# Performance work log

Hardware: AMD Instinct MI355X
Metric: run time of the kernel (lower is better)

## Reference

```python
import jax, jax.numpy as jnp
import numpy as np

NEG_SLOPE = 0.2  # PyG GATConv default negative_slope


def gat_conv(x, W, a_src, a_dst, bias, src, dst, heads, out_c, concat):
    """PyG-style GATConv with self-loops. x:[N,F_in], W:[F_in,heads*out_c]."""
    N = x.shape[0]
    # add self loops
    loop = jnp.arange(N, dtype=src.dtype)
    src = jnp.concatenate([src, loop])
    dst = jnp.concatenate([dst, loop])
    h = (x @ W).reshape(N, heads, out_c)            # [N,H,C]
    alpha_src = jnp.sum(h * a_src, axis=-1)          # [N,H]
    alpha_dst = jnp.sum(h * a_dst, axis=-1)          # [N,H]
    e = jax.nn.leaky_relu(alpha_src[src] + alpha_dst[dst], NEG_SLOPE)  # [E,H]
    # segment softmax over incoming edges of each destination node
    m = jax.ops.segment_max(e, dst, num_segments=N)  # [N,H]
    ex = jnp.exp(e - m[dst])
    s = jax.ops.segment_sum(ex, dst, num_segments=N)
    alpha = ex / (s[dst] + 1e-16)                    # [E,H]
    msg = h[src] * alpha[:, :, None]                 # [E,H,C]
    out = jax.ops.segment_sum(msg, dst, num_segments=N)  # [N,H,C]
    out = out.reshape(N, heads * out_c) if concat else out.mean(axis=1)
    return out + bias


def setup_inputs() -> dict:
    key = jax.random.key(0)
    ks = jax.random.split(key, 16)
    N, E = 25000, 400000
    node_dim, hidden, out_dim, heads = 64, 128, 256, 4

    def glorot(k, shape):
        fan = shape[0] + shape[-1]
        return jax.random.normal(k, shape, jnp.float32) * np.sqrt(2.0 / fan)

    return {
        "x": jax.random.normal(ks[0], (N, node_dim), jnp.float32),
        "edge_index": jax.random.randint(ks[1], (2, E), 0, N, jnp.int32),
        "W_emb": glorot(ks[2], (node_dim, hidden)),
        "b_emb": jnp.zeros((hidden,), jnp.float32),
        "W1": glorot(ks[3], (hidden, heads * hidden)),
        "a1_src": glorot(ks[4], (heads, hidden)),
        "a1_dst": glorot(ks[5], (heads, hidden)),
        "b1": jnp.zeros((heads * hidden,), jnp.float32),
        "W2": glorot(ks[6], (heads * hidden, hidden)),
        "a2_src": glorot(ks[7], (1, hidden)),
        "a2_dst": glorot(ks[8], (1, hidden)),
        "b2": jnp.zeros((hidden,), jnp.float32),
        "W_out": glorot(ks[9], (hidden, out_dim)),
        "b_out": jnp.zeros((out_dim,), jnp.float32),
    }


def reference(x, edge_index, W_emb, b_emb, W1, a1_src, a1_dst, b1, W2, a2_src, a2_dst, b2, W_out, b_out):
    src, dst = edge_index[0], edge_index[1]
    heads, hidden = a1_src.shape[0], a1_src.shape[1]
    h = jax.nn.relu(x @ W_emb + b_emb)                 # dropout is identity in eval
    h = gat_conv(h, W1, a1_src, a1_dst, b1, src, dst, heads, hidden, True)
    h = jax.nn.elu(h)
    h = gat_conv(h, W2, a2_src, a2_dst, b2, src, dst, 1, hidden, False)
    h = jax.nn.elu(h)
    g = jnp.mean(h, axis=0, keepdims=True)             # global mean pool, batch=None -> [1, hidden]
    return g @ W_out + b_out                           # [1, out_dim]
```

## Files before the change

kernel.cpp:

```cpp
#include <hip/hip_runtime.h>
#include <hip/hip_bf16.h>


#define LRELU(x) ((x) > 0.f ? (x) : 0.2f * (x))

typedef short bf16x8 __attribute__((ext_vector_type(8)));
typedef float f32x4 __attribute__((ext_vector_type(4)));
typedef float f32x2 __attribute__((ext_vector_type(2)));

static __device__ __forceinline__ unsigned short f2b(float f) {
    union { float f; unsigned u; } x; x.f = f;
    unsigned r = x.u + 0x7fff + ((x.u >> 16) & 1);
    return (unsigned short)(r >> 16);
}
static __device__ __forceinline__ float rl_f(float v, int c) {
    return __int_as_float(__builtin_amdgcn_readlane(__float_as_int(v), c));
}
static __device__ __forceinline__ unsigned char f2fp8(float v) {
    int p = __builtin_amdgcn_cvt_pk_fp8_f32(v, v, 0, false);
    return (unsigned char)(p & 0xff);
}

__global__ void zero_kernel(int* __restrict__ deg, float* __restrict__ pool,
                            int* __restrict__ done, int* __restrict__ flg,
                            int* __restrict__ agg, int N, int nb) {
    int i = blockIdx.x * blockDim.x + threadIdx.x;
    if (i < N) { deg[i] = 0; return; }
    i -= N;
    if (i < 128) { pool[i] = 0.f; return; }
    i -= 128;
    if (i == 0) { *done = 0; return; }
    i -= 1;
    if (i < nb) { flg[i] = 0; return; }
    i -= nb;
    if (i < nb) agg[i] = 0;
}

__global__ void degcount_prep(const int* __restrict__ ei, int E, int N,
                              int* __restrict__ deg, int blocksE,
                              const float* __restrict__ x, const float* __restrict__ We,
                              const float* __restrict__ W1, const float* __restrict__ W2,
                              unsigned short* __restrict__ xbS, unsigned short* __restrict__ WeS,
                              unsigned short* __restrict__ W1S, unsigned short* __restrict__ W2T,
                              int Nx) {
    if ((int)blockIdx.x < blocksE) {
        int i = blockIdx.x * blockDim.x + threadIdx.x;
        if (i < E) atomicAdd(&deg[ei[E + i]], 1);
        else if (i < E + N) atomicAdd(&deg[i - E], 1);
        return;
    }
    int i = (blockIdx.x - blocksE) * blockDim.x + threadIdx.x;
    if (i < Nx) {
        int r = i >> 6, k = i & 63;
        xbS[(r >> 4) * 1024 + (k >> 3) * 128 + (r & 15) * 8 + (k & 7)] = f2b(x[i]);
        return;
    }
    i -= Nx;
    if (i < 64 * 128) {
        int k = i >> 7, n = i & 127;
        WeS[(n >> 4) * 1024 + (k >> 5) * 512 + ((k >> 3) & 3) * 128 + (n & 15) * 8 + (k & 7)] = f2b(We[i]);
        return;
    }
    i -= 64 * 128;
    if (i < 128 * 512) {
        int k = i >> 9, n = i & 511;
        W1S[(n >> 4) * 2048 + (k >> 5) * 512 + ((k >> 3) & 3) * 128 + (n & 15) * 8 + (k & 7)] = f2b(W1[i]);
        return;
    }
    i -= 128 * 512;
    if (i < 512 * 128) { int k = i >> 7, n = i & 127; W2T[n * 512 + k] = f2b(W2[i]); return; }
}

__global__ __launch_bounds__(256) void scan_lookback(const int* __restrict__ deg,
                                                     int* __restrict__ rowptr,
                                                     int* __restrict__ cursor,
                                                     int* __restrict__ agg,
                                                     int* __restrict__ flg,
                                                     int N, int nb) {
    __shared__ int sd[256];
    __shared__ int soff;
    int t = threadIdx.x, b = blockIdx.x;
    int i = b * 256 + t;
    int d = (i < N) ? deg[i] : 0;
    sd[t] = d;
    __syncthreads();
    for (int off = 1; off < 256; off <<= 1) {
        int v = (t >= off) ? sd[t - off] : 0;
        __syncthreads();
        sd[t] += v;
        __syncthreads();
    }
    int incl = sd[t];
    int btot = sd[255];
    if (t == 0) {
        soff = 0;
        __hip_atomic_store(&agg[b], btot, __ATOMIC_RELAXED, __HIP_MEMORY_SCOPE_AGENT);
        __hip_atomic_store(&flg[b], 1, __ATOMIC_RELEASE, __HIP_MEMORY_SCOPE_AGENT);
    }
    if (b > 0 && t < 64) {
        int acc = 0;
        for (int p = t; p < b; p += 64) {
            while (__hip_atomic_load(&flg[p], __ATOMIC_ACQUIRE, __HIP_MEMORY_SCOPE_AGENT) == 0)
                __builtin_amdgcn_s_sleep(1);
            acc += __hip_atomic_load(&agg[p], __ATOMIC_RELAXED, __HIP_MEMORY_SCOPE_AGENT);
        }
#pragma unroll
        for (int o = 32; o >= 1; o >>= 1) acc += __shfl_xor(acc, o);
        if (t == 0) soff = acc;
    }
    __syncthreads();
    int off = soff;
    int excl = off + incl - d;
    if (i < N) { rowptr[i] = excl; cursor[i] = excl; }
    if (b == nb - 1 && t == 255) rowptr[N] = off + btot;
}

__global__ void scatter_kernel(const int* __restrict__ ei, int E, int N,
                               int* __restrict__ cursor, int* __restrict__ esrc) {
    int i = blockIdx.x * blockDim.x + threadIdx.x;
    int s, d;
    if (i < E) { s = ei[i]; d = ei[E + i]; }
    else if (i < E + N) { s = i - E; d = s; }
    else return;
    int pos = atomicAdd(&cursor[d], 1);
    esrc[pos] = s;
}

__global__ __launch_bounds__(256, 3) void gemm12_fused(const unsigned short* __restrict__ xbS,
                                                       const unsigned short* __restrict__ WeS,
                                                       const float* __restrict__ b_emb,
                                                       const unsigned short* __restrict__ W1S,
                                                       unsigned char* __restrict__ C8,
                                                       const float* __restrict__ a_src,
                                                       const float* __restrict__ a_dst,
                                                       float* __restrict__ as_out,
                                                       float* __restrict__ ad_out, int M) {
    __shared__ __align__(16) unsigned short h0s[128 * 132];
    __shared__ float sAl[128][2];

    int tid = threadIdx.x;
    int bx = blockIdx.x, by = blockIdx.y;
    int gm0 = by * 128, gn0 = bx * 128;
    int w = tid >> 6, lane = tid & 63;
    int wrow = (w >> 1) * 64, wc = w & 1, wcol = wc * 64;
    int l15 = lane & 15, quad = lane >> 4;

    f32x4 acc[4][4];
#pragma unroll
    for (int i = 0; i < 4; i++)
#pragma unroll
        for (int j = 0; j < 4; j++) acc[i][j] = {0.f, 0.f, 0.f, 0.f};

    const unsigned short* xA = xbS + (size_t)((gm0 + wrow) >> 4) * 1024 + quad * 128 + l15 * 8;
    const unsigned short* wB = WeS + (size_t)(wc * 4) * 1024 + quad * 128 + l15 * 8;
    const unsigned short* w1B = W1S + (size_t)(bx * 8 + wc * 4) * 2048 + quad * 128 + l15 * 8;
#pragma unroll
    for (int ks = 0; ks < 2; ks++) {
        bf16x8 af[4], bfr[4];
#pragma unroll
        for (int i = 0; i < 4; i++) af[i] = *(const bf16x8*)(xA + i * 1024 + ks * 512);
#pragma unroll
        for (int j = 0; j < 4; j++) bfr[j] = *(const bf16x8*)(wB + j * 1024 + ks * 512);
#pragma unroll
        for (int i = 0; i < 4; i++)
#pragma unroll
            for (int j = 0; j < 4; j++)
                acc[i][j] = __builtin_amdgcn_mfma_f32_16x16x32_bf16(af[i], bfr[j], acc[i][j], 0, 0, 0);
    }

    bf16x8 wp[4][4];
#pragma unroll
    for (int ks = 0; ks < 4; ks++)
#pragma unroll
        for (int j = 0; j < 4; j++)
            wp[ks][j] = *(const bf16x8*)(w1B + j * 2048 + ks * 512);

#pragma unroll
    for (int j = 0; j < 4; j++) {
        int col = wcol + j * 16 + l15;
        float bv = b_emb[col];
#pragma unroll
        for (int i = 0; i < 4; i++) {
            int row = wrow + i * 16 + quad * 4;
#pragma unroll
            for (int r = 0; r < 4; r++) {
                float v = fmaxf(acc[i][j][r] + bv, 0.f);
                h0s[(row + r) * 132 + col] = f2b(v);
            }
        }
    }
#pragma unroll
    for (int i = 0; i < 4; i++)
#pragma unroll
        for (int j = 0; j < 4; j++) acc[i][j] = {0.f, 0.f, 0.f, 0.f};
    __syncthreads();

#pragma unroll
    for (int ks = 0; ks < 4; ks++) {
        bf16x8 af[4];
#pragma unroll
        for (int i = 0; i < 4; i++)
            af[i] = *(const bf16x8*)&h0s[(wrow + i * 16 + l15) * 132 + ks * 32 + quad * 8];
#pragma unroll
        for (int i = 0; i < 4; i++)
#pragma unroll
            for (int j = 0; j < 4; j++)
                acc[i][j] = __builtin_amdgcn_mfma_f32_16x16x32_bf16(af[i], wp[ks][j], acc[i][j], 0, 0, 0);
    }

#pragma unroll
    for (int i = 0; i < 4; i++) {
        int row = gm0 + wrow + i * 16 + quad * 4;
#pragma unroll
        for (int j = 0; j < 4; j++) {
            int col = gn0 + wcol + j * 16 + l15;
#pragma unroll
            for (int r = 0; r < 4; r++) {
                int gr = row + r;
                if (gr < M) C8[(size_t)gr * 512 + col] = f2fp8(acc[i][j][r]);
            }
        }
    }

    {
        int hh = bx;
        float as_c[4], ad_c[4];
#pragma unroll
        for (int j = 0; j < 4; j++) {
            int c = gn0 + wcol + j * 16 + l15;
            as_c[j] = a_src[c];
            ad_c[j] = a_dst[c];
        }
#pragma unroll
        for (int i = 0; i < 4; i++) {
#pragma unroll
            for (int r = 0; r < 4; r++) {
                float ps = 0.f, pd = 0.f;
#pragma unroll
                for (int j = 0; j < 4; j++) {
                    ps += acc[i][j][r] * as_c[j];
                    pd += acc[i][j][r] * ad_c[j];
                }
#pragma unroll
                for (int o = 1; o < 16; o <<= 1) {
                    ps += __shfl_xor(ps, o);
                    pd += __shfl_xor(pd, o);
                }
                if (wcol == 64 && l15 == 0) {
                    int lr = wrow + i * 16 + quad * 4 + r;
                    sAl[lr][0] = ps;
                    sAl[lr][1] = pd;
                }
            }
        }
        __syncthreads();
        if (wcol == 0) {
#pragma unroll
            for (int i = 0; i < 4; i++) {
#pragma unroll
                for (int r = 0; r < 4; r++) {
                    float ps = 0.f, pd = 0.f;
#pragma unroll
                    for (int j = 0; j < 4; j++) {
                        ps += acc[i][j][r] * as_c[j];
                        pd += acc[i][j][r] * ad_c[j];
                    }
#pragma unroll
                    for (int o = 1; o < 16; o <<= 1) {
                        ps += __shfl_xor(ps, o);
                        pd += __shfl_xor(pd, o);
                    }
                    if (l15 == 0) {
                        int lr = wrow + i * 16 + quad * 4 + r;
                        int gr = gm0 + lr;
                        if (gr < M) {
                            as_out[(size_t)gr * 4 + hh] = ps + sAl[lr][0];
                            ad_out[(size_t)gr * 4 + hh] = pd + sAl[lr][1];
                        }
                    }
                }
            }
        }
    }
}

template <int ACT, int OFMT, int ALPHA, int H>
__global__ __launch_bounds__(256) void gemm_mfma_nt(const unsigned short* __restrict__ A,
                                                    const unsigned short* __restrict__ Bt,
                                                    const float* __restrict__ bias,
                                                    void* __restrict__ Cout,
                                                    const float* __restrict__ a_src,
                                                    const float* __restrict__ a_dst,
                                                    float* __restrict__ as_out,
                                                    float* __restrict__ ad_out,
                                                    int M, int N, int K) {
    __shared__ __align__(16) unsigned short As[128 * 40];
    __shared__ __align__(16) unsigned short Bs[128 * 40];
    __shared__ float sAl[128][2];
    int tid = threadIdx.x;
    int gm0 = blockIdx.y * 128, gn0 = blockIdx.x * 128;
    int w = tid >> 6, lane = tid & 63;
    int wrow = (w >> 1) * 64, wcol = (w & 1) * 64;
    int l15 = lane & 15, quad = lane >> 4;

    f32x4 acc[4][4];
#pragma unroll
    for (int i = 0; i < 4; i++)
#pragma unroll
        for (int j = 0; j < 4; j++) acc[i][j] = {0.f, 0.f, 0.f, 0.f};

    for (int k0 = 0; k0 < K; k0 += 32) {
#pragma unroll
        for (int rr = 0; rr < 2; rr++) {
            int lin = tid + rr * 256;
            int row = lin >> 2;
            int cg = (lin & 3) * 8;
            int grow = gm0 + row; if (grow >= M) grow = M - 1;
            uint4 va = *(const uint4*)&A[(size_t)grow * K + k0 + cg];
            *(uint4*)&As[row * 40 + cg] = va;
            uint4 vb = *(const uint4*)&Bt[(size_t)(gn0 + row) * K + k0 + cg];
            *(uint4*)&Bs[row * 40 + cg] = vb;
        }
        __syncthreads();
        bf16x8 af[4], bfr[4];
#pragma unroll
        for (int i = 0; i < 4; i++) {
            af[i]  = *(const bf16x8*)&As[(wrow + i * 16 + l15) * 40 + quad * 8];
            bfr[i] = *(const bf16x8*)&Bs[(wcol + i * 16 + l15) * 40 + quad * 8];
        }
#pragma unroll
        for (int i = 0; i < 4; i++)
#pragma unroll
            for (int j = 0; j < 4; j++)
                acc[i][j] = __builtin_amdgcn_mfma_f32_16x16x32_bf16(af[i], bfr[j], acc[i][j], 0, 0, 0);
        __syncthreads();
    }

    if (OFMT == 0) {
        unsigned short* C = (unsigned short*)Cout;
#pragma unroll
        for (int i = 0; i < 4; i++) {
            int row = gm0 + wrow + i * 16 + quad * 4;
#pragma unroll
            for (int j = 0; j < 4; j++) {
                int col = gn0 + wcol + j * 16 + l15;
                float bv = bias ? bias[col] : 0.f;
#pragma unroll
                for (int r = 0; r < 4; r++) {
                    int gr = row + r;
                    if (gr < M) {
                        float v = acc[i][j][r] + bv;
                        if (ACT == 1) v = fmaxf(v, 0.f);
                        C[(size_t)gr * N + col] = f2b(v);
                    }
                }
            }
        }
    } else {
        unsigned char* C8 = (unsigned char*)Cout;
#pragma unroll
        for (int i = 0; i < 4; i++) {
            int row = gm0 + wrow + i * 16 + quad * 4;
#pragma unroll
            for (int j = 0; j < 4; j++) {
                int col = gn0 + wcol + j * 16 + l15;
#pragma unroll
                for (int r = 0; r < 4; r++) {
                    int gr = row + r;
                    if (gr < M) C8[(size_t)gr * N + col] = f2fp8(acc[i][j][r]);
                }
            }
        }
    }

    if (ALPHA) {
        int hh = blockIdx.x;
        float as_c[4], ad_c[4];
#pragma unroll
        for (int j = 0; j < 4; j++) {
            int c = gn0 + wcol + j * 16 + l15;
            as_c[j] = a_src[c];
            ad_c[j] = a_dst[c];
        }
#pragma unroll
        for (int i = 0; i < 4; i++) {
#pragma unroll
            for (int r = 0; r < 4; r++) {
                float ps = 0.f, pd = 0.f;
#pragma unroll
                for (int j = 0; j < 4; j++) {
                    ps += acc[i][j][r] * as_c[j];
                    pd += acc[i][j][r] * ad_c[j];
                }
#pragma unroll
                for (int o = 1; o < 16; o <<= 1) {
                    ps += __shfl_xor(ps, o);
                    pd += __shfl_xor(pd, o);
                }
                if (wcol == 64 && l15 == 0) {
                    int lr = wrow + i * 16 + quad * 4 + r;
                    sAl[lr][0] = ps;
                    sAl[lr][1] = pd;
                }
            }
        }
        __syncthreads();
        if (wcol == 0) {
#pragma unroll
            for (int i = 0; i < 4; i++) {
#pragma unroll
                for (int r = 0; r < 4; r++) {
                    float ps = 0.f, pd = 0.f;
#pragma unroll
                    for (int j = 0; j < 4; j++) {
                        ps += acc[i][j][r] * as_c[j];
                        pd += acc[i][j][r] * ad_c[j];
                    }
#pragma unroll
                    for (int o = 1; o < 16; o <<= 1) {
                        ps += __shfl_xor(ps, o);
                        pd += __shfl_xor(pd, o);
                    }
                    if (l15 == 0) {
                        int lr = wrow + i * 16 + quad * 4 + r;
                        int gr = gm0 + lr;
                        if (gr < M) {
                            as_out[(size_t)gr * H + hh] = ps + sAl[lr][0];
                            ad_out[(size_t)gr * H + hh] = pd + sAl[lr][1];
                        }
                    }
                }
            }
        }
    }
}

__global__ __launch_bounds__(256) void gat_agg_l1(const unsigned* __restrict__ hq,
                                                  const float4* __restrict__ as4,
                                                  const float4* __restrict__ ad4,
                                                  const int* __restrict__ rowptr,
                                                  const int* __restrict__ esrc,
                                                  const float* __restrict__ bias,
                                                  unsigned short* __restrict__ out, int N) {
    __shared__ float wlds_all[4][256];
    int w = threadIdx.x >> 6, lane = threadIdx.x & 63;
    int n = blockIdx.x * 4 + w;
    if (n >= N) return;
    float* wlds = wlds_all[w];
    int2 rp = *(const int2*)&rowptr[n];
    int begin = rp.x, deg = rp.y - rp.x;
    float4 adn = ad4[n];

    int s_l0 = 0;
    float4 e0 = {-3.4e38f, -3.4e38f, -3.4e38f, -3.4e38f};
    if (lane < deg) {
        s_l0 = esrc[begin + lane];
        float4 u = as4[s_l0];
        e0.x = LRELU(u.x + adn.x); e0.y = LRELU(u.y + adn.y);
        e0.z = LRELU(u.z + adn.z); e0.w = LRELU(u.w + adn.w);
    }
    float4 m = e0;
    for (int base = 64; base < deg; base += 64) {
        int j = base + lane;
        if (j < deg) {
            float4 u = as4[esrc[begin + j]];
            m.x = fmaxf(m.x, LRELU(u.x + adn.x)); m.y = fmaxf(m.y, LRELU(u.y + adn.y));
            m.z = fmaxf(m.z, LRELU(u.z + adn.z)); m.w = fmaxf(m.w, LRELU(u.w + adn.w));
        }
    }
#pragma unroll
    for (int o = 32; o >= 1; o >>= 1) {
        m.x = fmaxf(m.x, __shfl_xor(m.x, o));
        m.y = fmaxf(m.y, __shfl_xor(m.y, o));
        m.z = fmaxf(m.z, __shfl_xor(m.z, o));
        m.w = fmaxf(m.w, __shfl_xor(m.w, o));
    }
    float4 s4 = {0.f, 0.f, 0.f, 0.f};
    if (lane < deg) {
        s4.x = __expf(e0.x - m.x); s4.y = __expf(e0.y - m.y);
        s4.z = __expf(e0.z - m.z); s4.w = __expf(e0.w - m.w);
    }
    for (int base = 64; base < deg; base += 64) {
        int j = base + lane;
        if (j < deg) {
            float4 u = as4[esrc[begin + j]];
            s4.x += __expf(LRELU(u.x + adn.x) - m.x); s4.y += __expf(LRELU(u.y + adn.y) - m.y);
            s4.z += __expf(LRELU(u.z + adn.z) - m.z); s4.w += __expf(LRELU(u.w + adn.w) - m.w);
        }
    }
#pragma unroll
    for (int o = 32; o >= 1; o >>= 1) {
        s4.x += __shfl_xor(s4.x, o); s4.y += __shfl_xor(s4.y, o);
        s4.z += __shfl_xor(s4.z, o); s4.w += __shfl_xor(s4.w, o);
    }
    float4 inv = {1.f / (s4.x + 1e-16f), 1.f / (s4.y + 1e-16f),
                  1.f / (s4.z + 1e-16f), 1.f / (s4.w + 1e-16f)};

    f32x2 acc2[4] = {};
    int h = lane >> 4;
#define ACC_E1(q, wgt) { \
    f32x2 wv = {wgt, wgt}; \
    acc2[0] += wv * __builtin_amdgcn_cvt_pk_f32_fp8((int)q.x, false); \
    acc2[1] += wv * __builtin_amdgcn_cvt_pk_f32_fp8((int)q.x, true);  \
    acc2[2] += wv * __builtin_amdgcn_cvt_pk_f32_fp8((int)q.y, false); \
    acc2[3] += wv * __builtin_amdgcn_cvt_pk_f32_fp8((int)q.y, true);  }

    for (int base = 0; base < deg; base += 64) {
        int j = base + lane;
        int len = min(64, deg - base);
        int s_l = s_l0;
        float4 e = e0;
        if (base > 0 && j < deg) {
            s_l = esrc[begin + j];
            float4 u = as4[s_l];
            e.x = LRELU(u.x + adn.x); e.y = LRELU(u.y + adn.y);
            e.z = LRELU(u.z + adn.z); e.w = LRELU(u.w + adn.w);
        }
        if (j < deg) {
            float4 wv4 = {__expf(e.x - m.x) * inv.x, __expf(e.y - m.y) * inv.y,
                          __expf(e.z - m.z) * inv.z, __expf(e.w - m.w) * inv.w};
            *(float4*)&wlds[lane * 4] = wv4;
        }
        int c = 0;
        for (; c + 4 <= len; c += 4) {
            int s0 = __builtin_amdgcn_readlane(s_l, c);
            int s1 = __builtin_amdgcn_readlane(s_l, c + 1);
            int s2 = __builtin_amdgcn_readlane(s_l, c + 2);
            int s3 = __builtin_amdgcn_readlane(s_l, c + 3);
            uint2 q0 = *((const uint2*)(hq + (size_t)s0 * 128) + lane);
            uint2 q1 = *((const uint2*)(hq + (size_t)s1 * 128) + lane);
            uint2 q2 = *((const uint2*)(hq + (size_t)s2 * 128) + lane);
            uint2 q3 = *((const uint2*)(hq + (size_t)s3 * 128) + lane);
            float w0 = wlds[c * 4 + h];
            float w1 = wlds[c * 4 + 4 + h];
            float w2 = wlds[c * 4 + 8 + h];
            float w3 = wlds[c * 4 + 12 + h];
            ACC_E1(q0, w0); ACC_E1(q1, w1); ACC_E1(q2, w2); ACC_E1(q3, w3);
        }
        for (; c < len; c++) {
            int s0 = __builtin_amdgcn_readlane(s_l, c);
            uint2 q0 = *((const uint2*)(hq + (size_t)s0 * 128) + lane);
            float w0 = wlds[c * 4 + h];
            ACC_E1(q0, w0);
        }
    }
#undef ACC_E1
    int f0 = lane * 8;
    unsigned pk[4];
#pragma unroll
    for (int k = 0; k < 4; k++) {
        float v0 = acc2[k].x + bias[f0 + 2 * k];
        float v1 = acc2[k].y + bias[f0 + 2 * k + 1];
        v0 = v0 > 0.f ? v0 : (__expf(v0) - 1.f);
        v1 = v1 > 0.f ? v1 : (__expf(v1) - 1.f);
        pk[k] = (unsigned)f2b(v0) | ((unsigned)f2b(v1) << 16);
    }
    uint4 pv = {pk[0], pk[1], pk[2], pk[3]};
    *((uint4*)(out + (size_t)n * 512) + lane) = pv;
}

__global__ __launch_bounds__(256) void gat_agg_l2(const unsigned char* __restrict__ hq,
                                                  const float* __restrict__ as,
                                                  const float* __restrict__ ad,
                                                  const int* __restrict__ rowptr,
                                                  const int* __restrict__ esrc,
                                                  const float* __restrict__ bias,
                                                  float* __restrict__ out, int N) {
    int w = threadIdx.x >> 6, lane = threadIdx.x & 63;
    int n = blockIdx.x * 4 + w;
    if (n >= N) return;
    int2 rp = *(const int2*)&rowptr[n];
    int begin = rp.x, deg = rp.y - rp.x;
    float adn = ad[n];

    int s_l0 = 0;
    float e0 = -3.4e38f;
    if (lane < deg) {
        s_l0 = esrc[begin + lane];
        e0 = LRELU(as[s_l0] + adn);
    }
    float m = e0;
    for (int base = 64; base < deg; base += 64) {
        int j = base + lane;
        if (j < deg) m = fmaxf(m, LRELU(as[esrc[begin + j]] + adn));
    }
#pragma unroll
    for (int o = 32; o >= 1; o >>= 1) m = fmaxf(m, __shfl_xor(m, o));

    float s = (lane < deg) ? __expf(e0 - m) : 0.f;
    for (int base = 64; base < deg; base += 64) {
        int j = base + lane;
        if (j < deg) s += __expf(LRELU(as[esrc[begin + j]] + adn) - m);
    }
#pragma unroll
    for (int o = 32; o >= 1; o >>= 1) s += __shfl_xor(s, o);
    float inv = 1.f / (s + 1e-16f);

    f32x2 acc2 = {0.f, 0.f};
    for (int base = 0; base < deg; base += 64) {
        int j = base + lane;
        int len = min(64, deg - base);
        int s_l = s_l0;
        float e = e0;
        if (base > 0 && j < deg) {
            s_l = esrc[begin + j];
            e = LRELU(as[s_l] + adn);
        }
        float w_l = (j < deg) ? __expf(e - m) * inv : 0.f;
        int c = 0;
        for (; c + 4 <= len; c += 4) {
            int sp0 = __builtin_amdgcn_readlane(s_l, c);
            int sp1 = __builtin_amdgcn_readlane(s_l, c + 1);
            int sp2 = __builtin_amdgcn_readlane(s_l, c + 2);
            int sp3 = __builtin_amdgcn_readlane(s_l, c + 3);
            unsigned short u0 = *((const unsigned short*)(hq + (size_t)sp0 * 128) + lane);
            unsigned short u1 = *((const unsigned short*)(hq + (size_t)sp1 * 128) + lane);
            unsigned short u2 = *((const unsigned short*)(hq + (size_t)sp2 * 128) + lane);
            unsigned short u3 = *((const unsigned short*)(hq + (size_t)sp3 * 128) + lane);
            float w0 = rl_f(w_l, c), w1 = rl_f(w_l, c + 1);
            float w2 = rl_f(w_l, c + 2), w3 = rl_f(w_l, c + 3);
            f32x2 wv0 = {w0, w0}, wv1 = {w1, w1}, wv2 = {w2, w2}, wv3 = {w3, w3};
            acc2 += wv0 * __builtin_amdgcn_cvt_pk_f32_fp8((int)u0, false);
            acc2 += wv1 * __builtin_amdgcn_cvt_pk_f32_fp8((int)u1, false);
            acc2 += wv2 * __builtin_amdgcn_cvt_pk_f32_fp8((int)u2, false);
            acc2 += wv3 * __builtin_amdgcn_cvt_pk_f32_fp8((int)u3, false);
        }
        for (; c < len; c++) {
            int sp0 = __builtin_amdgcn_readlane(s_l, c);
            float w0 = rl_f(w_l, c);
            unsigned short u0 = *((const unsigned short*)(hq + (size_t)sp0 * 128) + lane);
            f32x2 wv0 = {w0, w0};
            acc2 += wv0 * __builtin_amdgcn_cvt_pk_f32_fp8((int)u0, false);
        }
    }
    float v0 = acc2.x + bias[lane * 2];
    float v1 = acc2.y + bias[lane * 2 + 1];
    v0 = v0 > 0.f ? v0 : (__expf(v0) - 1.f);
    v1 = v1 > 0.f ? v1 : (__expf(v1) - 1.f);
    float2 pv = {v0, v1};
    *(float2*)&out[(size_t)n * 128 + lane * 2] = pv;
}

__global__ __launch_bounds__(256) void pool_final_kernel(const float* __restrict__ o2,
                                                         float* __restrict__ pool,
                                                         int* __restrict__ done,
                                                         const float* __restrict__ Wout,
                                                         const float* __restrict__ bout,
                                                         float* __restrict__ out,
                                                         int N, int nblocks, float invN) {
    __shared__ float4 sred[256];
    int f4 = threadIdx.x & 31;
    int r = blockIdx.x * 256 + (threadIdx.x >> 5);
    float4 acc = {0.f, 0.f, 0.f, 0.f};
    for (int i = 0; i < 32; i++, r += 8) {
        if (r < N) {
            float4 v = *(const float4*)&o2[(size_t)r * 128 + f4 * 4];
            acc.x += v.x; acc.y += v.y; acc.z += v.z; acc.w += v.w;
        }
    }
    sred[threadIdx.x] = acc;
    __syncthreads();
    if (threadIdx.x < 32) {
        float4 t = sred[threadIdx.x];
#pragma unroll
        for (int k = 1; k < 8; k++) {
            float4 u = sred[threadIdx.x + 32 * k];
            t.x += u.x; t.y += u.y; t.z += u.z; t.w += u.w;
        }
        atomicAdd(&pool[f4 * 4 + 0], t.x);
        atomicAdd(&pool[f4 * 4 + 1], t.y);
        atomicAdd(&pool[f4 * 4 + 2], t.z);
        atomicAdd(&pool[f4 * 4 + 3], t.w);
    }
    __threadfence();
    __shared__ int isLast;
    if (threadIdx.x == 0) isLast = (atomicAdd(done, 1) == nblocks - 1);
    __syncthreads();
    if (isLast) {
        __shared__ float spool[128];
        if (threadIdx.x < 128) spool[threadIdx.x] = atomicAdd(&pool[threadIdx.x], 0.f);
        __syncthreads();
        int o = threadIdx.x;
        float a = 0.f;
        for (int k = 0; k < 128; k++) a += spool[k] * Wout[k * 256 + o];
        out[o] = a * invN + bout[o];
    }
}

extern "C" void kernel_launch(void* const* d_in, const int* in_sizes, int n_in,
                              void* d_out, int out_size, void* d_ws, size_t ws_size,
                              hipStream_t stream) {
    const float* x      = (const float*)d_in[0];
    const int*   ei     = (const int*)d_in[1];
    const float* W_emb  = (const float*)d_in[2];
    const float* b_emb  = (const float*)d_in[3];
    const float* W1     = (const float*)d_in[4];
    const float* a1_src = (const float*)d_in[5];
    const float* a1_dst = (const float*)d_in[6];
    const float* b1     = (const float*)d_in[7];
    const float* W2     = (const float*)d_in[8];
    const float* a2_src = (const float*)d_in[9];
    const float* a2_dst = (const float*)d_in[10];
    const float* b2     = (const float*)d_in[11];
    const float* W_out  = (const float*)d_in[12];
    const float* b_out  = (const float*)d_in[13];
    float* out = (float*)d_out;

    const int N = in_sizes[0] / 64;
    const int E = in_sizes[1] / 2;
    const int Etot = E + N;
    const int nb = (N + 255) / 256;
    const int mtiles = (N + 127) / 128;
    const int nrb = mtiles * 8;

    char* ws = (char*)d_ws;
    size_t off = 0;
    auto alloc = [&](size_t bytes) -> void* {
        void* p = ws + off;
        off = (off + bytes + 255) & ~(size_t)255;
        return p;
    };
    typedef unsigned short u16;
    u16* xbS   = (u16*)alloc((size_t)nrb * 1024 * 2);
    u16* WeS   = (u16*)alloc((size_t)8 * 1024 * 2);
    u16* W1S   = (u16*)alloc((size_t)32 * 2048 * 2);
    u16* W2T   = (u16*)alloc((size_t)128 * 512 * 2);
    unsigned char* h1q = (unsigned char*)alloc((size_t)N * 512);
    u16* o1b   = (u16*)alloc((size_t)N * 512 * 2);
    unsigned char* h2q = (unsigned char*)alloc((size_t)N * 128);
    float* o2  = (float*)alloc((size_t)N * 128 * 4);
    float* as1 = (float*)alloc((size_t)N * 4 * 4);
    float* ad1 = (float*)alloc((size_t)N * 4 * 4);
    float* as2 = (float*)alloc((size_t)N * 4);
    float* ad2 = (float*)alloc((size_t)N * 4);
    float* pool = (float*)alloc(128 * 4);
    int* done   = (int*)alloc(256);
    int* rowptr = (int*)alloc((size_t)(N + 1) * 4);
    int* deg    = (int*)alloc((size_t)N * 4);
    int* cursor = (int*)alloc((size_t)N * 4);
    int* sagg   = (int*)alloc((size_t)nb * 4);
    int* sflg   = (int*)alloc((size_t)nb * 4);
    int* esrc   = (int*)alloc((size_t)Etot * 4);

    const int blocksE = (Etot + 255) / 256;
    const int Nx = N * 64;
    const int prepElems = Nx + 64 * 128 + 128 * 512 + 512 * 128;
    const int prepBlocks = (prepElems + 255) / 256;

    int zn = N + 128 + 1 + 2 * nb;
    zero_kernel<<<(zn + 255) / 256, 256, 0, stream>>>(deg, pool, done, sflg, sagg, N, nb);

    degcount_prep<<<blocksE + prepBlocks, 256, 0, stream>>>(ei, E, N, deg, blocksE,
                                                            x, W_emb, W1, W2,
                                                            xbS, WeS, W1S, W2T, Nx);

    scan_lookback<<<nb, 256, 0, stream>>>(deg, rowptr, cursor, sagg, sflg, N, nb);

    scatter_kernel<<<blocksE, 256, 0, stream>>>(ei, E, N, cursor, esrc);

    gemm12_fused<<<dim3(4, mtiles), 256, 0, stream>>>(xbS, WeS, b_emb, W1S, h1q,
                                                      a1_src, a1_dst, as1, ad1, N);

    gat_agg_l1<<<(N + 3) / 4, 256, 0, stream>>>((const unsigned*)h1q, (const float4*)as1,
                                                (const float4*)ad1, rowptr, esrc, b1, o1b, N);

    gemm_mfma_nt<0, 1, 1, 1><<<dim3(1, mtiles), 256, 0, stream>>>(
        o1b, W2T, nullptr, h2q, a2_src, a2_dst, as2, ad2, N, 128, 512);

    gat_agg_l2<<<(N + 3) / 4, 256, 0, stream>>>(h2q, as2, ad2, rowptr, esrc, b2, o2, N);

    int npb = (N + 255) / 256;
    pool_final_kernel<<<npb, 256, 0, stream>>>(o2, pool, done, W_out, b_out, out,
                                               N, npb, 1.f / (float)N);
}
```

Before: 269.0 us.

## Replace LDS-tiled layer-2 GEMM with direct-load 64-row MFMA kernel

The generic 128x128 LDS-staged GEMM used for layer 2 (K=512, N=128) is replaced by a specialised kernel. It loads bf16 fragments straight from global memory into registers with no LDS staging or per-k barriers, and uses 64-row tiles to double the block count. The fp8 output and the fused attention-logit epilogue are kept. This removes the shared-memory round trip and syncthreads overhead, and spreads the work over more blocks on a small GEMM. In exchange, B fragments are re-read from global/L2 by every wave instead of being shared through LDS.

Measured after the change: 274.3 us. No clear change (+2.0%).

```diff
diff --git a/kernel.cpp b/kernel.cpp
--- a/kernel.cpp
+++ b/kernel.cpp
@@ -284,106 +284,74 @@
     }
 }
 
-template <int ACT, int OFMT, int ALPHA, int H>
-__global__ __launch_bounds__(256) void gemm_mfma_nt(const unsigned short* __restrict__ A,
+__global__ __launch_bounds__(256) void gemm2_direct(const unsigned short* __restrict__ A,
                                                     const unsigned short* __restrict__ Bt,
-                                                    const float* __restrict__ bias,
-                                                    void* __restrict__ Cout,
+                                                    unsigned char* __restrict__ C8,
                                                     const float* __restrict__ a_src,
                                                     const float* __restrict__ a_dst,
                                                     float* __restrict__ as_out,
-                                                    float* __restrict__ ad_out,
-                                                    int M, int N, int K) {
-    __shared__ __align__(16) unsigned short As[128 * 40];
-    __shared__ __align__(16) unsigned short Bs[128 * 40];
-    __shared__ float sAl[128][2];
+                                                    float* __restrict__ ad_out, int M) {
+    __shared__ float sAl[64][2];
     int tid = threadIdx.x;
-    int gm0 = blockIdx.y * 128, gn0 = blockIdx.x * 128;
+    int gm0 = blockIdx.x * 64;
     int w = tid >> 6, lane = tid & 63;
-    int wrow = (w >> 1) * 64, wcol = (w & 1) * 64;
+    int wrow = (w >> 1) * 32, wc = w & 1, wcol = wc * 64;
     int l15 = lane & 15, quad = lane >> 4;
 
-    f32x4 acc[4][4];
-#pragma unroll
-    for (int i = 0; i < 4; i++)
+    f32x4 acc[2][4];
+#pragma unroll
+    for (int i = 0; i < 2; i++)
 #pragma unroll
         for (int j = 0; j < 4; j++) acc[i][j] = {0.f, 0.f, 0.f, 0.f};
 
-    for (int k0 = 0; k0 < K; k0 += 32) {
-#pragma unroll
-        for (int rr = 0; rr < 2; rr++) {
-            int lin = tid + rr * 256;
-            int row = lin >> 2;
-            int cg = (lin & 3) * 8;
-            int grow = gm0 + row; if (grow >= M) grow = M - 1;
-            uint4 va = *(const uint4*)&A[(size_t)grow * K + k0 + cg];
-            *(uint4*)&As[row * 40 + cg] = va;
-            uint4 vb = *(const uint4*)&Bt[(size_t)(gn0 + row) * K + k0 + cg];
-            *(uint4*)&Bs[row * 40 + cg] = vb;
-        }
-        __syncthreads();
-        bf16x8 af[4], bfr[4];
-#pragma unroll
-        for (int i = 0; i < 4; i++) {
-            af[i]  = *(const bf16x8*)&As[(wrow + i * 16 + l15) * 40 + quad * 8];
-            bfr[i] = *(const bf16x8*)&Bs[(wcol + i * 16 + l15) * 40 + quad * 8];
-        }
-#pragma unroll
-        for (int i = 0; i < 4; i++)
-#pragma unroll
-            for (int j = 0; j < 4; j++)
-                acc[i][j] = __builtin_amdgcn_mfma_f32_16x16x32_bf16(af[i], bfr[j], acc[i][j], 0, 0, 0);
-        __syncthreads();
-    }
-
-    if (OFMT == 0) {
-        unsigned short* C = (unsigned short*)Cout;
-#pragma unroll
-        for (int i = 0; i < 4; i++) {
-            int row = gm0 + wrow + i * 16 + quad * 4;
-#pragma unroll
-            for (int j = 0; j < 4; j++) {
-                int col = gn0 + wcol + j * 16 + l15;
-                float bv = bias ? bias[col] : 0.f;
-#pragma unroll
-                for (int r = 0; r < 4; r++) {
-                    int gr = row + r;
-                    if (gr < M) {
-                        float v = acc[i][j][r] + bv;
-                        if (ACT == 1) v = fmaxf(v, 0.f);
-                        C[(size_t)gr * N + col] = f2b(v);
-                    }
-                }
+    int r0 = gm0 + wrow + l15;      if (r0 >= M) r0 = M - 1;
+    int r1 = gm0 + wrow + 16 + l15; if (r1 >= M) r1 = M - 1;
+    const unsigned short* a0 = A + (size_t)r0 * 512 + quad * 8;
+    const unsigned short* a1 = A + (size_t)r1 * 512 + quad * 8;
+    const unsigned short* b0 = Bt + (size_t)(wcol + l15) * 512 + quad * 8;
+
+#pragma unroll 4
+    for (int ks = 0; ks < 16; ks++) {
+        bf16x8 af0 = *(const bf16x8*)(a0 + ks * 32);
+        bf16x8 af1 = *(const bf16x8*)(a1 + ks * 32);
+        bf16x8 bf0 = *(const bf16x8*)(b0 + ks * 32);
+        bf16x8 bf1 = *(const bf16x8*)(b0 + 16 * 512 + ks * 32);
+        bf16x8 bf2 = *(const bf16x8*)(b0 + 32 * 512 + ks * 32);
+        bf16x8 bf3 = *(const bf16x8*)(b0 + 48 * 512 + ks * 32);
+        acc[0][0] = __builtin_amdgcn_mfma_f32_16x16x32_bf16(af0, bf0, acc[0][0], 0, 0, 0);
+        acc[0][1] = __builtin_amdgcn_mfma_f32_16x16x32_bf16(af0, bf1, acc[0][1], 0, 0, 0);
+        acc[0][2] = __builtin_amdgcn_mfma_f32_16x16x32_bf16(af0, bf2, acc[0][2], 0, 0, 0);
+        acc[0][3] = __builtin_amdgcn_mfma_f32_16x16x32_bf16(af0, bf3, acc[0][3], 0, 0, 0);
+        acc[1][0] = __builtin_amdgcn_mfma_f32_16x16x32_bf16(af1, bf0, acc[1][0], 0, 0, 0);
+        acc[1][1] = __builtin_amdgcn_mfma_f32_16x16x32_bf16(af1, bf1, acc[1][1], 0, 0, 0);
+        acc[1][2] = __builtin_amdgcn_mfma_f32_16x16x32_bf16(af1, bf2, acc[1][2], 0, 0, 0);
+        acc[1][3] = __builtin_amdgcn_mfma_f32_16x16x32_bf16(af1, bf3, acc[1][3], 0, 0, 0);
+    }
+
+#pragma unroll
+    for (int i = 0; i < 2; i++) {
+        int row = gm0 + wrow + i * 16 + quad * 4;
+#pragma unroll
+        for (int j = 0; j < 4; j++) {
+            int col = wcol + j * 16 + l15;
+#pragma unroll
+            for (int r = 0; r < 4; r++) {
+                int gr = row + r;
+                if (gr < M) C8[(size_t)gr * 128 + col] = f2fp8(acc[i][j][r]);
             }
         }
-    } else {
-        unsigned char* C8 = (unsigned char*)Cout;
-#pragma unroll
-        for (int i = 0; i < 4; i++) {
-            int row = gm0 + wrow + i * 16 + quad * 4;
-#pragma unroll
-            for (int j = 0; j < 4; j++) {
-                int col = gn0 + wcol + j * 16 + l15;
-#pragma unroll
-                for (int r = 0; r < 4; r++) {
-                    int gr = row + r;
-                    if (gr < M) C8[(size_t)gr * N + col] = f2fp8(acc[i][j][r]);
-                }
-            }
-        }
-    }
-
-    if (ALPHA) {
-        int hh = blockIdx.x;
+    }
+
+    {
         float as_c[4], ad_c[4];
 #pragma unroll
         for (int j = 0; j < 4; j++) {
-            int c = gn0 + wcol + j * 16 + l15;
+            int c = wcol + j * 16 + l15;
             as_c[j] = a_src[c];
             ad_c[j] = a_dst[c];
         }
 #pragma unroll
-        for (int i = 0; i < 4; i++) {
+        for (int i = 0; i < 2; i++) {
 #pragma unroll
             for (int r = 0; r < 4; r++) {
                 float ps = 0.f, pd = 0.f;
@@ -407,7 +375,7 @@
         __syncthreads();
         if (wcol == 0) {
 #pragma unroll
-            for (int i = 0; i < 4; i++) {
+            for (int i = 0; i < 2; i++) {
 #pragma unroll
                 for (int r = 0; r < 4; r++) {
                     float ps = 0.f, pd = 0.f;
@@ -425,8 +393,8 @@
                         int lr = wrow + i * 16 + quad * 4 + r;
                         int gr = gm0 + lr;
                         if (gr < M) {
-                            as_out[(size_t)gr * H + hh] = ps + sAl[lr][0];
-                            ad_out[(size_t)gr * H + hh] = pd + sAl[lr][1];
+                            as_out[gr] = ps + sAl[lr][0];
+                            ad_out[gr] = pd + sAl[lr][1];
                         }
                     }
                 }
@@ -764,8 +732,8 @@
     gat_agg_l1<<<(N + 3) / 4, 256, 0, stream>>>((const unsigned*)h1q, (const float4*)as1,
                                                 (const float4*)ad1, rowptr, esrc, b1, o1b, N);
 
-    gemm_mfma_nt<0, 1, 1, 1><<<dim3(1, mtiles), 256, 0, stream>>>(
-        o1b, W2T, nullptr, h2q, a2_src, a2_dst, as2, ad2, N, 128, 512);
+    gemm2_direct<<<dim3((N + 63) / 64), 256, 0, stream>>>(
+        o1b, W2T, h2q, a2_src, a2_dst, as2, ad2, N);
 
     gat_agg_l2<<<(N + 3) / 4, 256, 0, stream>>>(h2q, as2, ad2, rowptr, esrc, b2, o2, N);
 
```
